# Performance work log

Measured on AMD Instinct MI355X. Metric: run time of the kernel, lower is better.

The kernel has to match this reference:

```python
import jax, jax.numpy as jnp
import numpy as np

D = 128   # embedding_dim
H = 256   # hidden_dim

def setup_inputs() -> dict:
    key = jax.random.key(0)
    ks = jax.random.split(key, 16)
    s = 0.02
    B, N = 4, 384
    inp = {
        "cities": jax.random.uniform(ks[0], (B, N, 2), dtype=jnp.float32),
        # city_encoder: Linear(2,H) -> ReLU -> Linear(H,D); weights stored [in,out]
        "We1": jax.random.normal(ks[1], (2, H), dtype=jnp.float32) * s,
        "be1": jnp.zeros((H,), jnp.float32),
        "We2": jax.random.normal(ks[2], (H, D), dtype=jnp.float32) * s,
        "be2": jnp.zeros((D,), jnp.float32),
        # attention: Linear(D,H) -> ReLU -> Linear(H,1)
        "Wa1": jax.random.normal(ks[3], (D, H), dtype=jnp.float32) * s,
        "ba1": jnp.zeros((H,), jnp.float32),
        "wa2": jax.random.normal(ks[4], (H, 1), dtype=jnp.float32) * s,
        "ba2": jnp.zeros((1,), jnp.float32),
        # decoder: Linear(2D,H) -> ReLU -> Linear(H,1) -> Sigmoid
        "Wd1": jax.random.normal(ks[5], (2 * D, H), dtype=jnp.float32) * s,
        "bd1": jnp.zeros((H,), jnp.float32),
        "wd2": jax.random.normal(ks[6], (H, 1), dtype=jnp.float32) * s,
        "bd2": jnp.zeros((1,), jnp.float32),
    }
    return inp


def reference(cities, We1, be1, We2, be2, Wa1, ba1, wa2, ba2, Wd1, bd1, wd2, bd2):
    B, N, _ = cities.shape
    # city encoder MLP: [B,N,2] -> [B,N,D]
    emb = jax.nn.relu(cities @ We1 + be1) @ We2 + be2
    # attention scores -> softmax over cities
    att = jax.nn.softmax((jax.nn.relu(emb @ Wa1 + ba1) @ wa2 + ba2).squeeze(-1), axis=1)
    # Pairwise decoder: concat(e_i, e_j) @ Wd1 == e_i @ Wd1[:D] + e_j @ Wd1[D:]
    Ai = emb @ Wd1[:D]   # [B,N,H] contribution of row city i
    Aj = emb @ Wd1[D:]   # [B,N,H] contribution of col city j
    h = jax.nn.relu(Ai[:, :, None, :] + Aj[:, None, :, :] + bd1)  # [B,N,N,H]
    p = jax.nn.sigmoid((h @ wd2).squeeze(-1) + bd2)               # [B,N,N]
    # diagonal (i == j) was never written in the torch loop -> stays 0
    p = p * (1.0 - jnp.eye(N, dtype=p.dtype))
    return att, p
```

## Files before the change

### kernel.cpp

```cpp
#include <hip/hip_runtime.h>
#include <hip/hip_fp16.h>

#define NCITY 384
#define BATCH 4
#define DIM   128
#define HID   256
#define M_TOT (BATCH * NCITY)
#define TR    3

__device__ __forceinline__ void chunk_stream(
    const float* __restrict__ W,
    const float (*emb_s)[DIM], float* scr, int tid, float outr[TR])
{
    const int c4 = tid & 63;
    const int wv = tid >> 6;
    const int k0 = wv * 32;

    float4 acc[TR];
    #pragma unroll
    for (int rr = 0; rr < TR; ++rr) acc[rr] = make_float4(0.f, 0.f, 0.f, 0.f);

    #pragma unroll 2
    for (int kb = 0; kb < 32; kb += 4) {
        float4 ev[TR];
        #pragma unroll
        for (int rr = 0; rr < TR; ++rr)
            ev[rr] = *(const float4*)&emb_s[rr][k0 + kb];
        #pragma unroll
        for (int kk = 0; kk < 4; ++kk) {
            const float4 w4 = *(const float4*)&W[(k0 + kb + kk) * HID + c4 * 4];
            #pragma unroll
            for (int rr = 0; rr < TR; ++rr) {
                const float e = ((const float*)&ev[rr])[kk];
                acc[rr].x = fmaf(e, w4.x, acc[rr].x);
                acc[rr].y = fmaf(e, w4.y, acc[rr].y);
                acc[rr].z = fmaf(e, w4.z, acc[rr].z);
                acc[rr].w = fmaf(e, w4.w, acc[rr].w);
            }
        }
    }
    __syncthreads();
    #pragma unroll
    for (int rr = 0; rr < TR; ++rr)
        *(float4*)&scr[(wv * TR + rr) * HID + c4 * 4] = acc[rr];
    __syncthreads();
    #pragma unroll
    for (int rr = 0; rr < TR; ++rr)
        outr[rr] = scr[(0 * TR + rr) * HID + tid] + scr[(1 * TR + rr) * HID + tid]
                 + scr[(2 * TR + rr) * HID + tid] + scr[(3 * TR + rr) * HID + tid];
}

__global__ __launch_bounds__(256, 2) void encoder_stream(
    const float* __restrict__ cities,
    const float* __restrict__ We1, const float* __restrict__ be1,
    const float* __restrict__ We2, const float* __restrict__ be2,
    const float* __restrict__ Wa1, const float* __restrict__ ba1,
    const float* __restrict__ wa2, const float* __restrict__ ba2,
    const float* __restrict__ Wd1, const float* __restrict__ bd1,
    float* __restrict__ score, float* __restrict__ Ai, float* __restrict__ Aj)
{
    __shared__ float h1_s[TR][HID];
    __shared__ float emb_s[TR][DIM];
    __shared__ float scr[4 * TR * HID];
    __shared__ float red2[4][TR];

    const int tid = threadIdx.x;
    const int r0  = blockIdx.x * TR;

    {
        const float w0 = We1[tid], w1 = We1[HID + tid], b1v = be1[tid];
        #pragma unroll
        for (int rr = 0; rr < TR; ++rr) {
            const float cxx = cities[(r0 + rr) * 2];
            const float cyy = cities[(r0 + rr) * 2 + 1];
            h1_s[rr][tid] = fmaxf(fmaf(cxx, w0, fmaf(cyy, w1, b1v)), 0.f);
        }
    }
    __syncthreads();

    {
        const int d4 = tid & 31;
        const int k0 = (tid >> 5) * 32;
        float4 acc[TR];
        #pragma unroll
        for (int rr = 0; rr < TR; ++rr) acc[rr] = make_float4(0.f, 0.f, 0.f, 0.f);

        #pragma unroll 2
        for (int kb = 0; kb < 32; kb += 4) {
            float4 hv[TR];
            #pragma unroll
            for (int rr = 0; rr < TR; ++rr)
                hv[rr] = *(const float4*)&h1_s[rr][k0 + kb];
            #pragma unroll
            for (int kk = 0; kk < 4; ++kk) {
                const float4 w4 = *(const float4*)&We2[(k0 + kb + kk) * DIM + d4 * 4];
                #pragma unroll
                for (int rr = 0; rr < TR; ++rr) {
                    const float h = ((const float*)&hv[rr])[kk];
                    acc[rr].x = fmaf(h, w4.x, acc[rr].x);
                    acc[rr].y = fmaf(h, w4.y, acc[rr].y);
                    acc[rr].z = fmaf(h, w4.z, acc[rr].z);
                    acc[rr].w = fmaf(h, w4.w, acc[rr].w);
                }
            }
        }
        #pragma unroll
        for (int rr = 0; rr < TR; ++rr) {
            acc[rr].x += __shfl_xor(acc[rr].x, 32);
            acc[rr].y += __shfl_xor(acc[rr].y, 32);
            acc[rr].z += __shfl_xor(acc[rr].z, 32);
            acc[rr].w += __shfl_xor(acc[rr].w, 32);
        }
        if ((tid & 63) < 32) {
            const int wv = tid >> 6;
            #pragma unroll
            for (int rr = 0; rr < TR; ++rr)
                *(float4*)&scr[(wv * TR + rr) * DIM + d4 * 4] = acc[rr];
        }
        __syncthreads();
        for (int o = tid; o < TR * DIM; o += 256) {
            const int rr = o >> 7, d = o & (DIM - 1);
            emb_s[rr][d] = scr[(0 * TR + rr) * DIM + d] + scr[(1 * TR + rr) * DIM + d]
                         + scr[(2 * TR + rr) * DIM + d] + scr[(3 * TR + rr) * DIM + d]
                         + be2[d];
        }
        __syncthreads();
    }

    float o6[TR];

    chunk_stream(Wa1, emb_s, scr, tid, o6);
    {
        const float ba1v = ba1[tid], wa2v = wa2[tid];
        const int wv = tid >> 6;
        #pragma unroll
        for (int rr = 0; rr < TR; ++rr) {
            float v = fmaxf(o6[rr] + ba1v, 0.f) * wa2v;
            #pragma unroll
            for (int off = 32; off > 0; off >>= 1)
                v += __shfl_down(v, off);
            if ((tid & 63) == 0) red2[wv][rr] = v;
        }
        __syncthreads();
        if (tid < TR)
            score[r0 + tid] = red2[0][tid] + red2[1][tid] + red2[2][tid] + red2[3][tid];
    }

    chunk_stream(Wd1, emb_s, scr, tid, o6);
    {
        const float bd1v = bd1[tid];
        #pragma unroll
        for (int rr = 0; rr < TR; ++rr)
            Ai[(r0 + rr) * HID + tid] = o6[rr] + bd1v;
    }

    chunk_stream(Wd1 + DIM * HID, emb_s, scr, tid, o6);
    #pragma unroll
    for (int rr = 0; rr < TR; ++rr)
        Aj[(r0 + rr) * HID + tid] = o6[rr];
    (void)ba2;
}

__device__ __forceinline__ unsigned pk_add(unsigned a, unsigned b) {
    unsigned r; asm("v_pk_add_f16 %0, %1, %2" : "=v"(r) : "v"(a), "v"(b)); return r;
}
__device__ __forceinline__ unsigned pk_max0(unsigned a) {
    unsigned r; asm("v_pk_max_f16 %0, %1, %2" : "=v"(r) : "v"(a), "v"(0u)); return r;
}
__device__ __forceinline__ unsigned pk_fma(unsigned a, unsigned b, unsigned c) {
    unsigned r; asm("v_pk_fma_f16 %0, %1, %2, %3" : "=v"(r) : "v"(a), "v"(b), "v"(c)); return r;
}
__device__ __forceinline__ unsigned pack2(float a, float b) {
    union { __half2 h2; unsigned u; } c;
    c.h2 = __float22half2_rn(make_float2(a, b));
    return c.u;
}
__device__ __forceinline__ float sum2(unsigned u) {
    union { unsigned u; __half2 h2; } c; c.u = u;
    return __low2float(c.h2) + __high2float(c.h2);
}
union H8 { float4 f4; unsigned u[4]; };

__global__ __launch_bounds__(256) void pair_sm_kernel(
    const float* __restrict__ Ai, const float* __restrict__ Aj,
    const float* __restrict__ wd2, const float* __restrict__ bd2,
    const float* __restrict__ score, float* __restrict__ att,
    float* __restrict__ p)
{
    const int tid = threadIdx.x;
    const int b   = blockIdx.y;

    if (blockIdx.x == 144) {
        __shared__ float red[8];
        const int t = tid;
        const float v0 = score[b * NCITY + t];
        const bool  h2v = (t < NCITY - 256);
        const float v1 = h2v ? score[b * NCITY + 256 + t] : -3.4e38f;
        float m = fmaxf(v0, v1);
        #pragma unroll
        for (int off = 32; off > 0; off >>= 1)
            m = fmaxf(m, __shfl_down(m, off));
        if ((t & 63) == 0) red[t >> 6] = m;
        __syncthreads();
        m = fmaxf(fmaxf(red[0], red[1]), fmaxf(red[2], red[3]));
        const float e0 = __expf(v0 - m);
        const float e1 = h2v ? __expf(v1 - m) : 0.f;
        float s = e0 + e1;
        #pragma unroll
        for (int off = 32; off > 0; off >>= 1)
            s += __shfl_down(s, off);
        if ((t & 63) == 0) red[4 + (t >> 6)] = s;
        __syncthreads();
        s = red[4] + red[5] + red[6] + red[7];
        att[b * NCITY + t] = e0 / s;
        if (h2v) att[b * NCITY + 256 + t] = e1 / s;
        return;
    }

    __shared__ __half ai_s[32 * HID];
    __shared__ __half aj_s[32 * HID];
    __shared__ unsigned wd2h[HID / 2];

    const int i0 = (blockIdx.x / 12) * 32;
    const int j0 = (blockIdx.x % 12) * 32;

    if (tid < HID / 2) {
        const float2 w2 = *(const float2*)&wd2[tid * 2];
        wd2h[tid] = pack2(w2.x, w2.y);
    }

    for (int u = tid; u < 32 * 32; u += 256) {
        const int r = u >> 5, s = u & 31;
        const int su = (s ^ (r & 15)) * 8;
        {
            const int g = (b * NCITY + i0 + r) * HID + s * 8;
            const float4 f0 = *(const float4*)&Ai[g];
            const float4 f1 = *(const float4*)&Ai[g + 4];
            H8 pk;
            pk.u[0] = pack2(f0.x, f0.y);
            pk.u[1] = pack2(f0.z, f0.w);
            pk.u[2] = pack2(f1.x, f1.y);
            pk.u[3] = pack2(f1.z, f1.w);
            *(float4*)&ai_s[r * HID + su] = pk.f4;
        }
        {
            const int g = (b * NCITY + j0 + r) * HID + s * 8;
            const float4 f0 = *(const float4*)&Aj[g];
            const float4 f1 = *(const float4*)&Aj[g + 4];
            H8 pk;
            pk.u[0] = pack2(f0.x, f0.y);
            pk.u[1] = pack2(f0.z, f0.w);
            pk.u[2] = pack2(f1.x, f1.y);
            pk.u[3] = pack2(f1.z, f1.w);
            *(float4*)&aj_s[r * HID + su] = pk.f4;
        }
    }
    __syncthreads();

    const int tx = tid & 15;
    const int ty = tid >> 4;

    unsigned a00A = 0u, a00B = 0u, a01A = 0u, a01B = 0u;
    unsigned a10A = 0u, a10B = 0u, a11A = 0u, a11B = 0u;

    #pragma unroll 4
    for (int k8 = 0; k8 < 32; ++k8) {
        const int ci = (k8 ^ ty) * 8;
        const int cj = (k8 ^ tx) * 8;
        H8 x0, x1, y0, y1;
        x0.f4 = *(const float4*)&ai_s[ ty       * HID + ci];
        x1.f4 = *(const float4*)&ai_s[(ty + 16) * HID + ci];
        y0.f4 = *(const float4*)&aj_s[ tx       * HID + cj];
        y1.f4 = *(const float4*)&aj_s[(tx + 16) * HID + cj];

        #pragma unroll
        for (int q = 0; q < 4; ++q) {
            const unsigned w = wd2h[k8 * 4 + q];
            const unsigned t00 = pk_max0(pk_add(x0.u[q], y0.u[q]));
            const unsigned t01 = pk_max0(pk_add(x0.u[q], y1.u[q]));
            const unsigned t10 = pk_max0(pk_add(x1.u[q], y0.u[q]));
            const unsigned t11 = pk_max0(pk_add(x1.u[q], y1.u[q]));
            if (q < 2) {
                a00A = pk_fma(t00, w, a00A);
                a01A = pk_fma(t01, w, a01A);
                a10A = pk_fma(t10, w, a10A);
                a11A = pk_fma(t11, w, a11A);
            } else {
                a00B = pk_fma(t00, w, a00B);
                a01B = pk_fma(t01, w, a01B);
                a10B = pk_fma(t10, w, a10B);
                a11B = pk_fma(t11, w, a11B);
            }
        }
    }

    const float bd = bd2[0];
    float accs[2][2];
    accs[0][0] = sum2(a00A) + sum2(a00B);
    accs[0][1] = sum2(a01A) + sum2(a01B);
    accs[1][0] = sum2(a10A) + sum2(a10B);
    accs[1][1] = sum2(a11A) + sum2(a11B);

    #pragma unroll
    for (int ii = 0; ii < 2; ++ii) {
        #pragma unroll
        for (int jj = 0; jj < 2; ++jj) {
            const int gi = i0 + ty + ii * 16;
            const int gj = j0 + tx + jj * 16;
            const float v = 1.f / (1.f + __expf(-(accs[ii][jj] + bd)));
            p[(b * NCITY + gi) * NCITY + gj] = (gi == gj) ? 0.f : v;
        }
    }
}

extern "C" void kernel_launch(void* const* d_in, const int* in_sizes, int n_in,
                              void* d_out, int out_size, void* d_ws, size_t ws_size,
                              hipStream_t stream)
{
    const float* cities = (const float*)d_in[0];
    const float* We1    = (const float*)d_in[1];
    const float* be1    = (const float*)d_in[2];
    const float* We2    = (const float*)d_in[3];
    const float* be2    = (const float*)d_in[4];
    const float* Wa1    = (const float*)d_in[5];
    const float* ba1    = (const float*)d_in[6];
    const float* wa2    = (const float*)d_in[7];
    const float* ba2    = (const float*)d_in[8];
    const float* Wd1    = (const float*)d_in[9];
    const float* bd1    = (const float*)d_in[10];
    const float* wd2    = (const float*)d_in[11];
    const float* bd2    = (const float*)d_in[12];

    float* out_att = (float*)d_out;
    float* out_p   = out_att + M_TOT;

    float* score = (float*)d_ws;
    float* Ai    = score + M_TOT;
    float* Aj    = Ai + M_TOT * HID;

    encoder_stream<<<M_TOT / TR, 256, 0, stream>>>(
        cities, We1, be1, We2, be2, Wa1, ba1, wa2, ba2, Wd1, bd1,
        score, Ai, Aj);

    pair_sm_kernel<<<dim3(145, BATCH), 256, 0, stream>>>(
        Ai, Aj, wd2, bd2, score, out_att, out_p);
}
```

Measured before the change: 33.28 us.

## Split encoder into tiled embedding and head GEMM kernels with fp16 outputs

Replaces the single per-3-row encoder kernel with two kernels. One computes embeddings with the We2 tile staged in shared memory. The other computes the attention and decoder head projections as tiled GEMMs over 16 rows by 128 columns, emitting partial attention scores and fp16 Ai/Aj directly. The pair kernel then loads the fp16 data without a conversion step and sums the two score partials. This aims to cut redundant weight reads and halve Ai/Aj traffic, at the cost of an extra kernel launch and an intermediate embedding round trip through global memory.

```diff
diff --git a/kernel.cpp b/kernel.cpp
--- a/kernel.cpp
+++ b/kernel.cpp
@@ -5,161 +5,9 @@
 #define BATCH 4
 #define DIM   128
 #define HID   256
-#define M_TOT (BATCH * NCITY)
-#define TR    3
-
-__device__ __forceinline__ void chunk_stream(
-    const float* __restrict__ W,
-    const float (*emb_s)[DIM], float* scr, int tid, float outr[TR])
-{
-    const int c4 = tid & 63;
-    const int wv = tid >> 6;
-    const int k0 = wv * 32;
-
-    float4 acc[TR];
-    #pragma unroll
-    for (int rr = 0; rr < TR; ++rr) acc[rr] = make_float4(0.f, 0.f, 0.f, 0.f);
-
-    #pragma unroll 2
-    for (int kb = 0; kb < 32; kb += 4) {
-        float4 ev[TR];
-        #pragma unroll
-        for (int rr = 0; rr < TR; ++rr)
-            ev[rr] = *(const float4*)&emb_s[rr][k0 + kb];
-        #pragma unroll
-        for (int kk = 0; kk < 4; ++kk) {
-            const float4 w4 = *(const float4*)&W[(k0 + kb + kk) * HID + c4 * 4];
-            #pragma unroll
-            for (int rr = 0; rr < TR; ++rr) {
-                const float e = ((const float*)&ev[rr])[kk];
-                acc[rr].x = fmaf(e, w4.x, acc[rr].x);
-                acc[rr].y = fmaf(e, w4.y, acc[rr].y);
-                acc[rr].z = fmaf(e, w4.z, acc[rr].z);
-                acc[rr].w = fmaf(e, w4.w, acc[rr].w);
-            }
-        }
-    }
-    __syncthreads();
-    #pragma unroll
-    for (int rr = 0; rr < TR; ++rr)
-        *(float4*)&scr[(wv * TR + rr) * HID + c4 * 4] = acc[rr];
-    __syncthreads();
-    #pragma unroll
-    for (int rr = 0; rr < TR; ++rr)
-        outr[rr] = scr[(0 * TR + rr) * HID + tid] + scr[(1 * TR + rr) * HID + tid]
-                 + scr[(2 * TR + rr) * HID + tid] + scr[(3 * TR + rr) * HID + tid];
-}
-
-__global__ __launch_bounds__(256, 2) void encoder_stream(
-    const float* __restrict__ cities,
-    const float* __restrict__ We1, const float* __restrict__ be1,
-    const float* __restrict__ We2, const float* __restrict__ be2,
-    const float* __restrict__ Wa1, const float* __restrict__ ba1,
-    const float* __restrict__ wa2, const float* __restrict__ ba2,
-    const float* __restrict__ Wd1, const float* __restrict__ bd1,
-    float* __restrict__ score, float* __restrict__ Ai, float* __restrict__ Aj)
-{
-    __shared__ float h1_s[TR][HID];
-    __shared__ float emb_s[TR][DIM];
-    __shared__ float scr[4 * TR * HID];
-    __shared__ float red2[4][TR];
-
-    const int tid = threadIdx.x;
-    const int r0  = blockIdx.x * TR;
-
-    {
-        const float w0 = We1[tid], w1 = We1[HID + tid], b1v = be1[tid];
-        #pragma unroll
-        for (int rr = 0; rr < TR; ++rr) {
-            const float cxx = cities[(r0 + rr) * 2];
-            const float cyy = cities[(r0 + rr) * 2 + 1];
-            h1_s[rr][tid] = fmaxf(fmaf(cxx, w0, fmaf(cyy, w1, b1v)), 0.f);
-        }
-    }
-    __syncthreads();
-
-    {
-        const int d4 = tid & 31;
-        const int k0 = (tid >> 5) * 32;
-        float4 acc[TR];
-        #pragma unroll
-        for (int rr = 0; rr < TR; ++rr) acc[rr] = make_float4(0.f, 0.f, 0.f, 0.f);
-
-        #pragma unroll 2
-        for (int kb = 0; kb < 32; kb += 4) {
-            float4 hv[TR];
-            #pragma unroll
-            for (int rr = 0; rr < TR; ++rr)
-                hv[rr] = *(const float4*)&h1_s[rr][k0 + kb];
-            #pragma unroll
-            for (int kk = 0; kk < 4; ++kk) {
-                const float4 w4 = *(const float4*)&We2[(k0 + kb + kk) * DIM + d4 * 4];
-                #pragma unroll
-                for (int rr = 0; rr < TR; ++rr) {
-                    const float h = ((const float*)&hv[rr])[kk];
-                    acc[rr].x = fmaf(h, w4.x, acc[rr].x);
-                    acc[rr].y = fmaf(h, w4.y, acc[rr].y);
-                    acc[rr].z = fmaf(h, w4.z, acc[rr].z);
-                    acc[rr].w = fmaf(h, w4.w, acc[rr].w);
-                }
-            }
-        }
-        #pragma unroll
-        for (int rr = 0; rr < TR; ++rr) {
-            acc[rr].x += __shfl_xor(acc[rr].x, 32);
-            acc[rr].y += __shfl_xor(acc[rr].y, 32);
-            acc[rr].z += __shfl_xor(acc[rr].z, 32);
-            acc[rr].w += __shfl_xor(acc[rr].w, 32);
-        }
-        if ((tid & 63) < 32) {
-            const int wv = tid >> 6;
-            #pragma unroll
-            for (int rr = 0; rr < TR; ++rr)
-                *(float4*)&scr[(wv * TR + rr) * DIM + d4 * 4] = acc[rr];
-        }
-        __syncthreads();
-        for (int o = tid; o < TR * DIM; o += 256) {
-            const int rr = o >> 7, d = o & (DIM - 1);
-            emb_s[rr][d] = scr[(0 * TR + rr) * DIM + d] + scr[(1 * TR + rr) * DIM + d]
-                         + scr[(2 * TR + rr) * DIM + d] + scr[(3 * TR + rr) * DIM + d]
-                         + be2[d];
-        }
-        __syncthreads();
-    }
-
-    float o6[TR];
-
-    chunk_stream(Wa1, emb_s, scr, tid, o6);
-    {
-        const float ba1v = ba1[tid], wa2v = wa2[tid];
-        const int wv = tid >> 6;
-        #pragma unroll
-        for (int rr = 0; rr < TR; ++rr) {
-            float v = fmaxf(o6[rr] + ba1v, 0.f) * wa2v;
-            #pragma unroll
-            for (int off = 32; off > 0; off >>= 1)
-                v += __shfl_down(v, off);
-            if ((tid & 63) == 0) red2[wv][rr] = v;
-        }
-        __syncthreads();
-        if (tid < TR)
-            score[r0 + tid] = red2[0][tid] + red2[1][tid] + red2[2][tid] + red2[3][tid];
-    }
-
-    chunk_stream(Wd1, emb_s, scr, tid, o6);
-    {
-        const float bd1v = bd1[tid];
-        #pragma unroll
-        for (int rr = 0; rr < TR; ++rr)
-            Ai[(r0 + rr) * HID + tid] = o6[rr] + bd1v;
-    }
-
-    chunk_stream(Wd1 + DIM * HID, emb_s, scr, tid, o6);
-    #pragma unroll
-    for (int rr = 0; rr < TR; ++rr)
-        Aj[(r0 + rr) * HID + tid] = o6[rr];
-    (void)ba2;
-}
+#define M_TOT 1536
+
+typedef unsigned short u16;
 
 __device__ __forceinline__ unsigned pk_add(unsigned a, unsigned b) {
     unsigned r; asm("v_pk_add_f16 %0, %1, %2" : "=v"(r) : "v"(a), "v"(b)); return r;
@@ -179,12 +27,175 @@
     union { unsigned u; __half2 h2; } c; c.u = u;
     return __low2float(c.h2) + __high2float(c.h2);
 }
+__device__ __forceinline__ u16 h_bits(float x) {
+    union { __half h; u16 s; } c;
+    c.h = __float2half(x);
+    return c.s;
+}
 union H8 { float4 f4; unsigned u[4]; };
 
+__global__ __launch_bounds__(256, 2) void emb_burst(
+    const float* __restrict__ cities,
+    const float* __restrict__ We1, const float* __restrict__ be1,
+    const float* __restrict__ We2, const float* __restrict__ be2,
+    float* __restrict__ emb)
+{
+    __shared__ float Bs[256 * 64];
+    __shared__ float h1[8 * 256];
+
+    const int tid = threadIdx.x;
+    const int d0  = blockIdx.x * 64;
+    const int r0  = blockIdx.y * 8;
+
+    const int c16 = tid & 15;
+    const int kr  = tid >> 4;
+    float4 breg[16];
+    #pragma unroll
+    for (int i = 0; i < 16; ++i)
+        breg[i] = *(const float4*)&We2[(kr + i * 16) * DIM + d0 + c16 * 4];
+
+    {
+        const float w0 = We1[tid], w1 = We1[HID + tid], b1v = be1[tid];
+        #pragma unroll
+        for (int r = 0; r < 8; ++r) {
+            const float cx = cities[(r0 + r) * 2];
+            const float cy = cities[(r0 + r) * 2 + 1];
+            h1[r * HID + tid] = fmaxf(fmaf(cx, w0, fmaf(cy, w1, b1v)), 0.f);
+        }
+    }
+    #pragma unroll
+    for (int i = 0; i < 16; ++i)
+        *(float4*)&Bs[(kr + i * 16) * 64 + c16 * 4] = breg[i];
+    __syncthreads();
+
+    const int r  = tid >> 5;
+    const int c2 = tid & 31;
+    float2 acc = {0.f, 0.f};
+    #pragma unroll 4
+    for (int k4 = 0; k4 < 64; ++k4) {
+        const float4 a4 = *(const float4*)&h1[r * HID + k4 * 4];
+        #pragma unroll
+        for (int kk = 0; kk < 4; ++kk) {
+            const float2 b = *(const float2*)&Bs[(k4 * 4 + kk) * 64 + c2 * 2];
+            const float a = (&a4.x)[kk];
+            acc.x = fmaf(a, b.x, acc.x);
+            acc.y = fmaf(a, b.y, acc.y);
+        }
+    }
+    const float2 be2v = *(const float2*)&be2[d0 + c2 * 2];
+    acc.x += be2v.x;
+    acc.y += be2v.y;
+    *(float2*)&emb[(r0 + r) * DIM + d0 + c2 * 2] = acc;
+}
+
+__global__ __launch_bounds__(256, 2) void heads_burst(
+    const float* __restrict__ emb,
+    const float* __restrict__ Wa1, const float* __restrict__ Wd1,
+    const float* __restrict__ ba1, const float* __restrict__ wa2,
+    const float* __restrict__ bd1,
+    float* __restrict__ score_part,
+    u16* __restrict__ Ai_u, u16* __restrict__ Aj_u)
+{
+    __shared__ float As[16 * 128];
+    __shared__ float Bs[128 * 128];
+
+    const int tid = threadIdx.x;
+    const int g   = blockIdx.x;
+    const int m0  = blockIdx.y * 16;
+
+    const float* Bsrc;
+    int c0;
+    if (g < 2)      { Bsrc = Wa1;             c0 = g * 128; }
+    else if (g < 4) { Bsrc = Wd1;             c0 = (g - 2) * 128; }
+    else            { Bsrc = Wd1 + DIM * HID; c0 = (g - 4) * 128; }
+
+    {
+        const int cq = tid & 31, kr = tid >> 5;
+        #pragma unroll
+        for (int i = 0; i < 16; ++i) {
+            const int k = kr + i * 8;
+            *(float4*)&Bs[k * 128 + cq * 4] =
+                *(const float4*)&Bsrc[k * HID + c0 + cq * 4];
+        }
+    }
+    {
+        const int r = tid & 15, q = tid >> 4;
+        #pragma unroll
+        for (int i = 0; i < 2; ++i) {
+            const int qq = q + i * 16;
+            *(float4*)&As[r * 128 + qq * 4] =
+                *(const float4*)&emb[(m0 + r) * DIM + qq * 4];
+        }
+    }
+    __syncthreads();
+
+    const int r  = tid >> 4;
+    const int cq = tid & 15;
+    float4 acc0 = {0.f, 0.f, 0.f, 0.f};
+    float4 acc1 = {0.f, 0.f, 0.f, 0.f};
+    #pragma unroll 4
+    for (int k4 = 0; k4 < 32; ++k4) {
+        const float4 a4 = *(const float4*)&As[r * 128 + k4 * 4];
+        #pragma unroll
+        for (int kk = 0; kk < 4; ++kk) {
+            const int k = k4 * 4 + kk;
+            const float a = (&a4.x)[kk];
+            const float4 b0 = *(const float4*)&Bs[k * 128 + cq * 4];
+            const float4 b1 = *(const float4*)&Bs[k * 128 + (cq + 16) * 4];
+            acc0.x = fmaf(a, b0.x, acc0.x);
+            acc0.y = fmaf(a, b0.y, acc0.y);
+            acc0.z = fmaf(a, b0.z, acc0.z);
+            acc0.w = fmaf(a, b0.w, acc0.w);
+            acc1.x = fmaf(a, b1.x, acc1.x);
+            acc1.y = fmaf(a, b1.y, acc1.y);
+            acc1.z = fmaf(a, b1.z, acc1.z);
+            acc1.w = fmaf(a, b1.w, acc1.w);
+        }
+    }
+
+    if (g < 2) {
+        const float4 ba0 = *(const float4*)&ba1[c0 + cq * 4];
+        const float4 ba1v = *(const float4*)&ba1[c0 + (cq + 16) * 4];
+        const float4 wa0 = *(const float4*)&wa2[c0 + cq * 4];
+        const float4 wa1v = *(const float4*)&wa2[c0 + (cq + 16) * 4];
+        float s = fmaxf(acc0.x + ba0.x, 0.f) * wa0.x
+                + fmaxf(acc0.y + ba0.y, 0.f) * wa0.y
+                + fmaxf(acc0.z + ba0.z, 0.f) * wa0.z
+                + fmaxf(acc0.w + ba0.w, 0.f) * wa0.w
+                + fmaxf(acc1.x + ba1v.x, 0.f) * wa1v.x
+                + fmaxf(acc1.y + ba1v.y, 0.f) * wa1v.y
+                + fmaxf(acc1.z + ba1v.z, 0.f) * wa1v.z
+                + fmaxf(acc1.w + ba1v.w, 0.f) * wa1v.w;
+        s += __shfl_xor(s, 1);
+        s += __shfl_xor(s, 2);
+        s += __shfl_xor(s, 4);
+        s += __shfl_xor(s, 8);
+        if (cq == 0)
+            score_part[g * M_TOT + m0 + r] = s;
+    } else {
+        u16* dst = (g < 4) ? Ai_u : Aj_u;
+        const int cc = (g < 4) ? (g - 2) * 128 : (g - 4) * 128;
+        float4 o0 = acc0, o1 = acc1;
+        if (g < 4) {
+            const float4 b0 = *(const float4*)&bd1[cc + cq * 4];
+            const float4 b1 = *(const float4*)&bd1[cc + (cq + 16) * 4];
+            o0.x += b0.x; o0.y += b0.y; o0.z += b0.z; o0.w += b0.w;
+            o1.x += b1.x; o1.y += b1.y; o1.z += b1.z; o1.w += b1.w;
+        }
+        uint2 p0, p1;
+        p0.x = (unsigned)h_bits(o0.x) | ((unsigned)h_bits(o0.y) << 16);
+        p0.y = (unsigned)h_bits(o0.z) | ((unsigned)h_bits(o0.w) << 16);
+        p1.x = (unsigned)h_bits(o1.x) | ((unsigned)h_bits(o1.y) << 16);
+        p1.y = (unsigned)h_bits(o1.z) | ((unsigned)h_bits(o1.w) << 16);
+        *(uint2*)&dst[(m0 + r) * HID + cc + cq * 4] = p0;
+        *(uint2*)&dst[(m0 + r) * HID + cc + (cq + 16) * 4] = p1;
+    }
+}
+
 __global__ __launch_bounds__(256) void pair_sm_kernel(
-    const float* __restrict__ Ai, const float* __restrict__ Aj,
+    const __half* __restrict__ Ai, const __half* __restrict__ Aj,
     const float* __restrict__ wd2, const float* __restrict__ bd2,
-    const float* __restrict__ score, float* __restrict__ att,
+    const float* __restrict__ sp, float* __restrict__ att,
     float* __restrict__ p)
 {
     const int tid = threadIdx.x;
@@ -193,9 +204,10 @@
     if (blockIdx.x == 144) {
         __shared__ float red[8];
         const int t = tid;
-        const float v0 = score[b * NCITY + t];
+        const float v0 = sp[b * NCITY + t] + sp[M_TOT + b * NCITY + t];
         const bool  h2v = (t < NCITY - 256);
-        const float v1 = h2v ? score[b * NCITY + 256 + t] : -3.4e38f;
+        const float v1 = h2v ? (sp[b * NCITY + 256 + t] + sp[M_TOT + b * NCITY + 256 + t])
+                             : -3.4e38f;
         float m = fmaxf(v0, v1);
         #pragma unroll
         for (int off = 32; off > 0; off >>= 1)
@@ -232,28 +244,10 @@
     for (int u = tid; u < 32 * 32; u += 256) {
         const int r = u >> 5, s = u & 31;
         const int su = (s ^ (r & 15)) * 8;
-        {
-            const int g = (b * NCITY + i0 + r) * HID + s * 8;
-            const float4 f0 = *(const float4*)&Ai[g];
-            const float4 f1 = *(const float4*)&Ai[g + 4];
-            H8 pk;
-            pk.u[0] = pack2(f0.x, f0.y);
-            pk.u[1] = pack2(f0.z, f0.w);
-            pk.u[2] = pack2(f1.x, f1.y);
-            pk.u[3] = pack2(f1.z, f1.w);
-            *(float4*)&ai_s[r * HID + su] = pk.f4;
-        }
-        {
-            const int g = (b * NCITY + j0 + r) * HID + s * 8;
-            const float4 f0 = *(const float4*)&Aj[g];
-            const float4 f1 = *(const float4*)&Aj[g + 4];
-            H8 pk;
-            pk.u[0] = pack2(f0.x, f0.y);
-            pk.u[1] = pack2(f0.z, f0.w);
-            pk.u[2] = pack2(f1.x, f1.y);
-            pk.u[3] = pack2(f1.z, f1.w);
-            *(float4*)&aj_s[r * HID + su] = pk.f4;
-        }
+        *(float4*)&ai_s[r * HID + su] =
+            *(const float4*)&Ai[(b * NCITY + i0 + r) * HID + s * 8];
+        *(float4*)&aj_s[r * HID + su] =
+            *(const float4*)&Aj[(b * NCITY + j0 + r) * HID + s * 8];
     }
     __syncthreads();
 
@@ -330,18 +324,23 @@
     const float* bd1    = (const float*)d_in[10];
     const float* wd2    = (const float*)d_in[11];
     const float* bd2    = (const float*)d_in[12];
+    (void)ba2;
 
     float* out_att = (float*)d_out;
     float* out_p   = out_att + M_TOT;
 
-    float* score = (float*)d_ws;
-    float* Ai    = score + M_TOT;
-    float* Aj    = Ai + M_TOT * HID;
-
-    encoder_stream<<<M_TOT / TR, 256, 0, stream>>>(
-        cities, We1, be1, We2, be2, Wa1, ba1, wa2, ba2, Wd1, bd1,
-        score, Ai, Aj);
+    float* score_part = (float*)d_ws;
+    float* emb        = score_part + 2 * M_TOT;
+    u16*   Ai_u       = (u16*)(emb + M_TOT * DIM);
+    u16*   Aj_u       = Ai_u + M_TOT * HID;
+
+    emb_burst<<<dim3(2, 192), 256, 0, stream>>>(
+        cities, We1, be1, We2, be2, emb);
+
+    heads_burst<<<dim3(6, 96), 256, 0, stream>>>(
+        emb, Wa1, Wd1, ba1, wa2, bd1, score_part, Ai_u, Aj_u);
 
     pair_sm_kernel<<<dim3(145, BATCH), 256, 0, stream>>>(
-        Ai, Aj, wd2, bd2, score, out_att, out_p);
-}
+        (const __half*)Ai_u, (const __half*)Aj_u, wd2, bd2,
+        score_part, out_att, out_p);
+}
```

After: 41.33 us. 24.2% more time.

## Rewrite encoder with fp16 MFMA tiles and emit fp16 Ai/Aj directly

Applied to the files above, without the earlier changes.

The encoder moves from fp32 scalar FMA over 3 rows per block (512 blocks) to fp16 MFMA 16x16x32 over 64 rows per block (24 blocks). Each block stages the weights into swizzled LDS as fp16. Ai and Aj are now written as fp16, so the pair kernel copies them straight into LDS without conversion, which also halves the intermediate traffic. The risks are only 24 blocks on a large GPU, each block re-converting all weight matrices, and extra fp16 rounding of the embedding and the hidden activations.

```diff
diff --git a/kernel.cpp b/kernel.cpp
--- a/kernel.cpp
+++ b/kernel.cpp
@@ -5,184 +5,202 @@
 #define BATCH 4
 #define DIM   128
 #define HID   256
-#define M_TOT (BATCH * NCITY)
-#define TR    3
-
-__device__ __forceinline__ void chunk_stream(
-    const float* __restrict__ W,
-    const float (*emb_s)[DIM], float* scr, int tid, float outr[TR])
-{
-    const int c4 = tid & 63;
-    const int wv = tid >> 6;
-    const int k0 = wv * 32;
-
-    float4 acc[TR];
-    #pragma unroll
-    for (int rr = 0; rr < TR; ++rr) acc[rr] = make_float4(0.f, 0.f, 0.f, 0.f);
-
-    #pragma unroll 2
-    for (int kb = 0; kb < 32; kb += 4) {
-        float4 ev[TR];
-        #pragma unroll
-        for (int rr = 0; rr < TR; ++rr)
-            ev[rr] = *(const float4*)&emb_s[rr][k0 + kb];
-        #pragma unroll
-        for (int kk = 0; kk < 4; ++kk) {
-            const float4 w4 = *(const float4*)&W[(k0 + kb + kk) * HID + c4 * 4];
-            #pragma unroll
-            for (int rr = 0; rr < TR; ++rr) {
-                const float e = ((const float*)&ev[rr])[kk];
-                acc[rr].x = fmaf(e, w4.x, acc[rr].x);
-                acc[rr].y = fmaf(e, w4.y, acc[rr].y);
-                acc[rr].z = fmaf(e, w4.z, acc[rr].z);
-                acc[rr].w = fmaf(e, w4.w, acc[rr].w);
-            }
-        }
-    }
-    __syncthreads();
-    #pragma unroll
-    for (int rr = 0; rr < TR; ++rr)
-        *(float4*)&scr[(wv * TR + rr) * HID + c4 * 4] = acc[rr];
-    __syncthreads();
-    #pragma unroll
-    for (int rr = 0; rr < TR; ++rr)
-        outr[rr] = scr[(0 * TR + rr) * HID + tid] + scr[(1 * TR + rr) * HID + tid]
-                 + scr[(2 * TR + rr) * HID + tid] + scr[(3 * TR + rr) * HID + tid];
-}
-
-__global__ __launch_bounds__(256, 2) void encoder_stream(
+#define M_TOT 1536
+
+typedef unsigned short u16;
+typedef _Float16 f16x8 __attribute__((ext_vector_type(8)));
+typedef float f32x4 __attribute__((ext_vector_type(4)));
+
+__device__ __forceinline__ unsigned pk_add(unsigned a, unsigned b) {
+    unsigned r; asm("v_pk_add_f16 %0, %1, %2" : "=v"(r) : "v"(a), "v"(b)); return r;
+}
+__device__ __forceinline__ unsigned pk_max0(unsigned a) {
+    unsigned r; asm("v_pk_max_f16 %0, %1, %2" : "=v"(r) : "v"(a), "v"(0u)); return r;
+}
+__device__ __forceinline__ unsigned pk_fma(unsigned a, unsigned b, unsigned c) {
+    unsigned r; asm("v_pk_fma_f16 %0, %1, %2, %3" : "=v"(r) : "v"(a), "v"(b), "v"(c)); return r;
+}
+__device__ __forceinline__ unsigned pack2(float a, float b) {
+    union { __half2 h2; unsigned u; } c;
+    c.h2 = __float22half2_rn(make_float2(a, b));
+    return c.u;
+}
+__device__ __forceinline__ float sum2(unsigned u) {
+    union { unsigned u; __half2 h2; } c; c.u = u;
+    return __low2float(c.h2) + __high2float(c.h2);
+}
+__device__ __forceinline__ u16 h_bits(float x) {
+    union { __half h; u16 s; } c;
+    c.h = __float2half(x);
+    return c.s;
+}
+union H8 { float4 f4; unsigned u[4]; };
+
+__global__ __launch_bounds__(256) void encoder_mfma(
     const float* __restrict__ cities,
     const float* __restrict__ We1, const float* __restrict__ be1,
     const float* __restrict__ We2, const float* __restrict__ be2,
     const float* __restrict__ Wa1, const float* __restrict__ ba1,
     const float* __restrict__ wa2, const float* __restrict__ ba2,
     const float* __restrict__ Wd1, const float* __restrict__ bd1,
-    float* __restrict__ score, float* __restrict__ Ai, float* __restrict__ Aj)
+    float* __restrict__ score, u16* __restrict__ Ai_u, u16* __restrict__ Aj_u)
 {
-    __shared__ float h1_s[TR][HID];
-    __shared__ float emb_s[TR][DIM];
-    __shared__ float scr[4 * TR * HID];
-    __shared__ float red2[4][TR];
+    __shared__ __align__(16) u16 A1[64 * 256];
+    __shared__ __align__(16) u16 Bs[32768];
+    __shared__ __align__(16) u16 A2[64 * 128];
+    __shared__ float cit_s[128];
+    __shared__ float be2_s[128];
+    __shared__ float score_s[64];
 
     const int tid = threadIdx.x;
-    const int r0  = blockIdx.x * TR;
+    const int w   = tid >> 6;
+    const int l   = tid & 63;
+    const int r0  = blockIdx.x * 64;
+
+    if (tid < 128) {
+        cit_s[tid] = cities[r0 * 2 + tid];
+        be2_s[tid] = be2[tid];
+    }
+
+    {
+        unsigned* B32 = (unsigned*)Bs;
+        #pragma unroll
+        for (int i = 0; i < 16; ++i) {
+            const int pidx = i * 256 + tid;
+            const int k2 = pidx >> 5;
+            const int n4 = pidx & 31;
+            const float4 w0 = ((const float4*)We2)[(2 * k2) * 32 + n4];
+            const float4 w1 = ((const float4*)We2)[(2 * k2 + 1) * 32 + n4];
+            #pragma unroll
+            for (int c = 0; c < 4; ++c) {
+                const int n = n4 * 4 + c;
+                const unsigned v = pack2((&w0.x)[c], (&w1.x)[c]);
+                B32[n * 64 + (((k2 >> 2) ^ (n & 15)) * 4) + (k2 & 3)] = v;
+            }
+        }
+    }
+    __syncthreads();
 
     {
         const float w0 = We1[tid], w1 = We1[HID + tid], b1v = be1[tid];
-        #pragma unroll
-        for (int rr = 0; rr < TR; ++rr) {
-            const float cxx = cities[(r0 + rr) * 2];
-            const float cyy = cities[(r0 + rr) * 2 + 1];
-            h1_s[rr][tid] = fmaxf(fmaf(cxx, w0, fmaf(cyy, w1, b1v)), 0.f);
+        #pragma unroll 8
+        for (int m = 0; m < 64; ++m) {
+            const float v = fmaxf(fmaf(cit_s[2 * m], w0,
+                                  fmaf(cit_s[2 * m + 1], w1, b1v)), 0.f);
+            A1[m * 256 + (((tid >> 3) ^ (m & 15)) * 8) + (tid & 7)] = h_bits(v);
         }
     }
     __syncthreads();
 
     {
-        const int d4 = tid & 31;
-        const int k0 = (tid >> 5) * 32;
-        float4 acc[TR];
-        #pragma unroll
-        for (int rr = 0; rr < TR; ++rr) acc[rr] = make_float4(0.f, 0.f, 0.f, 0.f);
+        const int mrow = w * 16 + (l & 15);
+        f16x8 af[8];
+        #pragma unroll
+        for (int kst = 0; kst < 8; ++kst)
+            af[kst] = *(const f16x8*)&A1[mrow * 256 + (((kst * 4 + (l >> 4)) ^ (l & 15)) * 8)];
+        #pragma unroll
+        for (int nt = 0; nt < 8; ++nt) {
+            f32x4 acc = {0.f, 0.f, 0.f, 0.f};
+            #pragma unroll
+            for (int kst = 0; kst < 8; ++kst) {
+                const f16x8 bf = *(const f16x8*)&Bs[(nt * 16 + (l & 15)) * 256
+                                    + (((kst * 4 + (l >> 4)) ^ (l & 15)) * 8)];
+                acc = __builtin_amdgcn_mfma_f32_16x16x32_f16(af[kst], bf, acc, 0, 0, 0);
+            }
+            const int col = nt * 16 + (l & 15);
+            #pragma unroll
+            for (int i = 0; i < 4; ++i) {
+                const int row = w * 16 + (l >> 4) * 4 + i;
+                const float v = acc[i] + be2_s[col];
+                A2[row * 128 + (((col >> 3) ^ (row & 15)) * 8) + (col & 7)] = h_bits(v);
+            }
+        }
+    }
+    __syncthreads();
+
+    float rs[4] = {0.f, 0.f, 0.f, 0.f};
+    const int mrow = w * 16 + (l & 15);
+
+    for (int ch = 0; ch < 3; ++ch) {
+        {
+            const float* src = (ch == 0) ? Wa1 : Wd1 + (ch - 1) * (DIM * HID);
+            unsigned* B32 = (unsigned*)Bs;
+            #pragma unroll
+            for (int i = 0; i < 16; ++i) {
+                const int pidx = i * 256 + tid;
+                const int k2 = pidx >> 6;
+                const int n4 = pidx & 63;
+                const float4 w0 = ((const float4*)src)[(2 * k2) * 64 + n4];
+                const float4 w1 = ((const float4*)src)[(2 * k2 + 1) * 64 + n4];
+                #pragma unroll
+                for (int c = 0; c < 4; ++c) {
+                    const int n = n4 * 4 + c;
+                    const unsigned v = pack2((&w0.x)[c], (&w1.x)[c]);
+                    B32[n * 32 + (((k2 >> 2) ^ (n & 15)) * 4) + (k2 & 3)] = v;
+                }
+            }
+        }
+        __syncthreads();
+
+        f16x8 a2f[4];
+        #pragma unroll
+        for (int kst = 0; kst < 4; ++kst)
+            a2f[kst] = *(const f16x8*)&A2[mrow * 128 + (((kst * 4 + (l >> 4)) ^ (l & 15)) * 8)];
 
         #pragma unroll 2
-        for (int kb = 0; kb < 32; kb += 4) {
-            float4 hv[TR];
-            #pragma unroll
-            for (int rr = 0; rr < TR; ++rr)
-                hv[rr] = *(const float4*)&h1_s[rr][k0 + kb];
-            #pragma unroll
-            for (int kk = 0; kk < 4; ++kk) {
-                const float4 w4 = *(const float4*)&We2[(k0 + kb + kk) * DIM + d4 * 4];
-                #pragma unroll
-                for (int rr = 0; rr < TR; ++rr) {
-                    const float h = ((const float*)&hv[rr])[kk];
-                    acc[rr].x = fmaf(h, w4.x, acc[rr].x);
-                    acc[rr].y = fmaf(h, w4.y, acc[rr].y);
-                    acc[rr].z = fmaf(h, w4.z, acc[rr].z);
-                    acc[rr].w = fmaf(h, w4.w, acc[rr].w);
+        for (int nt = 0; nt < 16; ++nt) {
+            f32x4 acc = {0.f, 0.f, 0.f, 0.f};
+            #pragma unroll
+            for (int kst = 0; kst < 4; ++kst) {
+                const f16x8 bf = *(const f16x8*)&Bs[(nt * 16 + (l & 15)) * 128
+                                    + (((kst * 4 + (l >> 4)) ^ (l & 15)) * 8)];
+                acc = __builtin_amdgcn_mfma_f32_16x16x32_f16(a2f[kst], bf, acc, 0, 0, 0);
+            }
+            const int col = nt * 16 + (l & 15);
+            if (ch == 0) {
+                const float ba = ba1[col], wa = wa2[col];
+                #pragma unroll
+                for (int i = 0; i < 4; ++i)
+                    rs[i] += fmaxf(acc[i] + ba, 0.f) * wa;
+            } else if (ch == 1) {
+                const float bd = bd1[col];
+                #pragma unroll
+                for (int i = 0; i < 4; ++i) {
+                    const int row = w * 16 + (l >> 4) * 4 + i;
+                    Ai_u[(r0 + row) * HID + col] = h_bits(acc[i] + bd);
                 }
-            }
-        }
-        #pragma unroll
-        for (int rr = 0; rr < TR; ++rr) {
-            acc[rr].x += __shfl_xor(acc[rr].x, 32);
-            acc[rr].y += __shfl_xor(acc[rr].y, 32);
-            acc[rr].z += __shfl_xor(acc[rr].z, 32);
-            acc[rr].w += __shfl_xor(acc[rr].w, 32);
-        }
-        if ((tid & 63) < 32) {
-            const int wv = tid >> 6;
-            #pragma unroll
-            for (int rr = 0; rr < TR; ++rr)
-                *(float4*)&scr[(wv * TR + rr) * DIM + d4 * 4] = acc[rr];
+            } else {
+                #pragma unroll
+                for (int i = 0; i < 4; ++i) {
+                    const int row = w * 16 + (l >> 4) * 4 + i;
+                    Aj_u[(r0 + row) * HID + col] = h_bits(acc[i]);
+                }
+            }
+        }
+
+        if (ch == 0) {
+            #pragma unroll
+            for (int i = 0; i < 4; ++i) {
+                rs[i] += __shfl_xor(rs[i], 1);
+                rs[i] += __shfl_xor(rs[i], 2);
+                rs[i] += __shfl_xor(rs[i], 4);
+                rs[i] += __shfl_xor(rs[i], 8);
+            }
+            if ((l & 15) == 0) {
+                #pragma unroll
+                for (int i = 0; i < 4; ++i)
+                    score_s[w * 16 + (l >> 4) * 4 + i] = rs[i];
+            }
         }
         __syncthreads();
-        for (int o = tid; o < TR * DIM; o += 256) {
-            const int rr = o >> 7, d = o & (DIM - 1);
-            emb_s[rr][d] = scr[(0 * TR + rr) * DIM + d] + scr[(1 * TR + rr) * DIM + d]
-                         + scr[(2 * TR + rr) * DIM + d] + scr[(3 * TR + rr) * DIM + d]
-                         + be2[d];
-        }
-        __syncthreads();
-    }
-
-    float o6[TR];
-
-    chunk_stream(Wa1, emb_s, scr, tid, o6);
-    {
-        const float ba1v = ba1[tid], wa2v = wa2[tid];
-        const int wv = tid >> 6;
-        #pragma unroll
-        for (int rr = 0; rr < TR; ++rr) {
-            float v = fmaxf(o6[rr] + ba1v, 0.f) * wa2v;
-            #pragma unroll
-            for (int off = 32; off > 0; off >>= 1)
-                v += __shfl_down(v, off);
-            if ((tid & 63) == 0) red2[wv][rr] = v;
-        }
-        __syncthreads();
-        if (tid < TR)
-            score[r0 + tid] = red2[0][tid] + red2[1][tid] + red2[2][tid] + red2[3][tid];
-    }
-
-    chunk_stream(Wd1, emb_s, scr, tid, o6);
-    {
-        const float bd1v = bd1[tid];
-        #pragma unroll
-        for (int rr = 0; rr < TR; ++rr)
-            Ai[(r0 + rr) * HID + tid] = o6[rr] + bd1v;
-    }
-
-    chunk_stream(Wd1 + DIM * HID, emb_s, scr, tid, o6);
-    #pragma unroll
-    for (int rr = 0; rr < TR; ++rr)
-        Aj[(r0 + rr) * HID + tid] = o6[rr];
+        if (ch == 0 && tid < 64)
+            score[r0 + tid] = score_s[tid];
+    }
     (void)ba2;
 }
 
-__device__ __forceinline__ unsigned pk_add(unsigned a, unsigned b) {
-    unsigned r; asm("v_pk_add_f16 %0, %1, %2" : "=v"(r) : "v"(a), "v"(b)); return r;
-}
-__device__ __forceinline__ unsigned pk_max0(unsigned a) {
-    unsigned r; asm("v_pk_max_f16 %0, %1, %2" : "=v"(r) : "v"(a), "v"(0u)); return r;
-}
-__device__ __forceinline__ unsigned pk_fma(unsigned a, unsigned b, unsigned c) {
-    unsigned r; asm("v_pk_fma_f16 %0, %1, %2, %3" : "=v"(r) : "v"(a), "v"(b), "v"(c)); return r;
-}
-__device__ __forceinline__ unsigned pack2(float a, float b) {
-    union { __half2 h2; unsigned u; } c;
-    c.h2 = __float22half2_rn(make_float2(a, b));
-    return c.u;
-}
-__device__ __forceinline__ float sum2(unsigned u) {
-    union { unsigned u; __half2 h2; } c; c.u = u;
-    return __low2float(c.h2) + __high2float(c.h2);
-}
-union H8 { float4 f4; unsigned u[4]; };
-
 __global__ __launch_bounds__(256) void pair_sm_kernel(
-    const float* __restrict__ Ai, const float* __restrict__ Aj,
+    const __half* __restrict__ Ai, const __half* __restrict__ Aj,
     const float* __restrict__ wd2, const float* __restrict__ bd2,
     const float* __restrict__ score, float* __restrict__ att,
     float* __restrict__ p)
@@ -232,28 +250,10 @@
     for (int u = tid; u < 32 * 32; u += 256) {
         const int r = u >> 5, s = u & 31;
         const int su = (s ^ (r & 15)) * 8;
-        {
-            const int g = (b * NCITY + i0 + r) * HID + s * 8;
-            const float4 f0 = *(const float4*)&Ai[g];
-            const float4 f1 = *(const float4*)&Ai[g + 4];
-            H8 pk;
-            pk.u[0] = pack2(f0.x, f0.y);
-            pk.u[1] = pack2(f0.z, f0.w);
-            pk.u[2] = pack2(f1.x, f1.y);
-            pk.u[3] = pack2(f1.z, f1.w);
-            *(float4*)&ai_s[r * HID + su] = pk.f4;
-        }
-        {
-            const int g = (b * NCITY + j0 + r) * HID + s * 8;
-            const float4 f0 = *(const float4*)&Aj[g];
-            const float4 f1 = *(const float4*)&Aj[g + 4];
-            H8 pk;
-            pk.u[0] = pack2(f0.x, f0.y);
-            pk.u[1] = pack2(f0.z, f0.w);
-            pk.u[2] = pack2(f1.x, f1.y);
-            pk.u[3] = pack2(f1.z, f1.w);
-            *(float4*)&aj_s[r * HID + su] = pk.f4;
-        }
+        *(float4*)&ai_s[r * HID + su] =
+            *(const float4*)&Ai[(b * NCITY + i0 + r) * HID + s * 8];
+        *(float4*)&aj_s[r * HID + su] =
+            *(const float4*)&Aj[(b * NCITY + j0 + r) * HID + s * 8];
     }
     __syncthreads();
 
@@ -335,13 +335,14 @@
     float* out_p   = out_att + M_TOT;
 
     float* score = (float*)d_ws;
-    float* Ai    = score + M_TOT;
-    float* Aj    = Ai + M_TOT * HID;
-
-    encoder_stream<<<M_TOT / TR, 256, 0, stream>>>(
+    u16*   Ai_u  = (u16*)(score + M_TOT);
+    u16*   Aj_u  = Ai_u + M_TOT * HID;
+
+    encoder_mfma<<<24, 256, 0, stream>>>(
         cities, We1, be1, We2, be2, Wa1, ba1, wa2, ba2, Wd1, bd1,
-        score, Ai, Aj);
+        score, Ai_u, Aj_u);
 
     pair_sm_kernel<<<dim3(145, BATCH), 256, 0, stream>>>(
-        Ai, Aj, wd2, bd2, score, out_att, out_p);
-}
+        (const __half*)Ai_u, (const __half*)Aj_u, wd2, bd2,
+        score, out_att, out_p);
+}
```

Result: slower. 50.81 us (+52.6%).
